# Performance work log

Hardware: AMD Instinct MI355X
Metric: run time of the kernel (lower is better)

Reference implementation:

```python
import jax, jax.numpy as jnp
import numpy as np

EPS = 1e-5


def _forward(fov, motion, video, timewindow,
             gru_w_ih, gru_w_hh, gru_b_ih, gru_b_hh,
             Wp, Wv_w, Wv_b, Wpv_w, Wpv_b,
             conv_w, conv_b, vbn_g, vbn_b,
             me_w, me_b, mbn_g, mbn_b):
    B, S, _ = fov.shape
    P = timewindow.shape[0]
    tot = B * S * P
    H = 784

    # ---- GRU (batch_first, 1 layer), PyTorch gate order r,z,n ----
    def step(h, x):  # h,x: [B,H],[B,528]
        gi = x @ gru_w_ih.T + gru_b_ih            # [B,3H]
        gh = h @ gru_w_hh.T + gru_b_hh
        i_r, i_z, i_n = jnp.split(gi, 3, axis=-1)
        h_r, h_z, h_n = jnp.split(gh, 3, axis=-1)
        r = jax.nn.sigmoid(i_r + h_r)
        z = jax.nn.sigmoid(i_z + h_z)
        n = jnp.tanh(i_n + r * h_n)
        h_new = (1.0 - z) * n + z * h
        return h_new, h_new

    h0 = jnp.zeros((B, H), dtype=fov.dtype)
    _, pref_seq = jax.lax.scan(step, h0, jnp.swapaxes(fov, 0, 1))  # [S,B,H]
    preference = jnp.swapaxes(pref_seq, 0, 1)                       # [B,S,H]

    # expand over P predictions -> [tot, 784]
    preference = jnp.broadcast_to(preference[:, :, None, :], (B, S, P, H)).reshape(tot, H)

    # ---- additive (Bahdanau) attention over 196 spatial locations ----
    p_att = preference @ Wp.T                                       # [tot,128]
    # attention keys: view video buffer as (tot,528,196), transpose
    v_key = jnp.swapaxes(video.reshape(tot, 528, 196), -2, -1)      # [tot,196,528]
    v_att = jnp.einsum('tnc,mc->tnm', v_key, Wv_w) + Wv_b           # [tot,196,128]
    v_att = jnp.tanh(v_att + p_att[:, None, :])
    scores = jnp.einsum('tnm,om->tno', v_att, Wpv_w)[..., 0] + Wpv_b[0]  # [tot,196]
    att = jax.nn.softmax(scores, axis=1)[..., None]                 # [tot,196,1]

    # weighted sum path: SAME buffer reinterpreted as (tot,196,528) (faithful to torch .view)
    vid = video.reshape(tot, 196, 528) * att                        # [tot,196,528]
    vid = jnp.swapaxes(vid, -2, -1)                                 # [tot,528,196]

    # 1x1 conv (528->4) + BatchNorm2d (batch stats) + ReLU
    vid = jnp.einsum('oc,tcn->ton', conv_w[:, :, 0, 0], vid) + conv_b[None, :, None]  # [tot,4,196]
    mu = jnp.mean(vid, axis=(0, 2), keepdims=True)
    var = jnp.var(vid, axis=(0, 2), keepdims=True)
    vid = (vid - mu) * jax.lax.rsqrt(var + EPS) * vbn_g[None, :, None] + vbn_b[None, :, None]
    vid = jax.nn.relu(vid).reshape(tot, 4 * 196)                    # [tot,784]

    # ---- motion branch: expand over P, Linear(90,128) + BatchNorm1d + ReLU ----
    mot = jnp.broadcast_to(motion[:, :, None, :, :], (B, S, P, 1, 90)).reshape(tot, 90)
    mot = mot @ me_w.T + me_b                                       # [tot,128]
    mmu = jnp.mean(mot, axis=0, keepdims=True)
    mvar = jnp.var(mot, axis=0, keepdims=True)
    mot = (mot - mmu) * jax.lax.rsqrt(mvar + EPS) * mbn_g + mbn_b
    mot = jax.nn.relu(mot)                                          # [tot,128]

    tw = jnp.broadcast_to(timewindow[None, :], (B * S, P)).reshape(tot, 1)
    return jnp.concatenate([tw, preference, mot, vid], axis=1)      # [tot,1697]


def setup_inputs() -> dict:
    key = jax.random.key(0)
    ks = jax.random.split(key, 24)
    B, S, P = 8, 32, 5
    C, H, M = 528, 784, 128

    def rn(k, shape, scale=0.05):
        return jax.random.normal(k, shape, dtype=jnp.float32) * scale

    return {
        'fov': rn(ks[0], (B, S, C), 1.0),
        'motion': rn(ks[1], (B, S, 1, 90), 1.0),
        'video': rn(ks[2], (B, S, P, C, 196), 1.0),
        'timewindow': jnp.arange(1, P + 1, dtype=jnp.float32),
        'gru_w_ih': rn(ks[3], (3 * H, C)),
        'gru_w_hh': rn(ks[4], (3 * H, H)),
        'gru_b_ih': rn(ks[5], (3 * H,)),
        'gru_b_hh': rn(ks[6], (3 * H,)),
        'Wp': rn(ks[7], (M, H)),
        'Wv_w': rn(ks[8], (M, C)),
        'Wv_b': rn(ks[9], (M,)),
        'Wpv_w': rn(ks[10], (1, M)),
        'Wpv_b': rn(ks[11], (1,)),
        'conv_w': rn(ks[12], (4, C, 1, 1)),
        'conv_b': rn(ks[13], (4,)),
        'vbn_g': jnp.ones((4,), jnp.float32),
        'vbn_b': jnp.zeros((4,), jnp.float32),
        'me_w': rn(ks[14], (M, 90)),
        'me_b': rn(ks[15], (M,)),
        'mbn_g': jnp.ones((M,), jnp.float32),
        'mbn_b': jnp.zeros((M,), jnp.float32),
    }


def reference(fov, motion, video, timewindow,
              gru_w_ih, gru_w_hh, gru_b_ih, gru_b_hh,
              Wp, Wv_w, Wv_b, Wpv_w, Wpv_b,
              conv_w, conv_b, vbn_g, vbn_b,
              me_w, me_b, mbn_g, mbn_b):
    return _forward(fov, motion, video, timewindow,
                    gru_w_ih, gru_w_hh, gru_b_ih, gru_b_hh,
                    Wp, Wv_w, Wv_b, Wpv_w, Wpv_b,
                    conv_w, conv_b, vbn_g, vbn_b,
                    me_w, me_b, mbn_g, mbn_b)
```

## Files before the change

### kernel.cpp

```cpp
#include <hip/hip_runtime.h>
#include <cfloat>
#include <cmath>


typedef __attribute__((ext_vector_type(8))) short short8;
typedef __attribute__((ext_vector_type(4))) float f32x4;

__device__ __forceinline__ unsigned bf16r(float f) {
  union { float f; unsigned u; } v;
  v.f = f;
  unsigned u = v.u;
  u += 0x7fffu + ((u >> 16) & 1u);
  return u >> 16;
}

__device__ __forceinline__ float tanh_fast(float x) {
  float e = __expf(2.f * x);
  return 1.f - 2.f / (e + 1.f);
}

#define GT_BM 32
#define GT_BN 64
#define GT_BK 16

__global__ __launch_bounds__(256) void gemm_nt(const float* __restrict__ A,
                                               const float* __restrict__ Bt,
                                               const float* __restrict__ bias,
                                               float* __restrict__ Cm,
                                               int Mn, int Nn, int Kn) {
  __shared__ float sA[GT_BM][GT_BK + 1];
  __shared__ float sB[GT_BK][68];
  const int tid = threadIdx.x;
  const int tm = tid >> 4;
  const int tn = tid & 15;
  const int rowBase = blockIdx.y * GT_BM;
  const int colBase = blockIdx.x * GT_BN;
  float acc[2][4] = {};

  for (int k0 = 0; k0 < Kn; k0 += GT_BK) {
    for (int u = tid; u < GT_BM * GT_BK; u += 256) {
      int r = u >> 4, kk = u & 15;
      int gk = k0 + kk, gr = rowBase + r;
      sA[r][kk] = (gr < Mn && gk < Kn) ? A[(size_t)gr * Kn + gk] : 0.f;
    }
    for (int u = tid; u < GT_BN * GT_BK; u += 256) {
      int n = u >> 4, kk = u & 15;
      int gk = k0 + kk, gn = colBase + n;
      sB[kk][n] = (gn < Nn && gk < Kn) ? Bt[(size_t)gn * Kn + gk] : 0.f;
    }
    __syncthreads();
#pragma unroll
    for (int kk = 0; kk < GT_BK; ++kk) {
      float a0 = sA[tm * 2 + 0][kk];
      float a1 = sA[tm * 2 + 1][kk];
      float b0 = sB[kk][tn * 4 + 0];
      float b1 = sB[kk][tn * 4 + 1];
      float b2 = sB[kk][tn * 4 + 2];
      float b3 = sB[kk][tn * 4 + 3];
      acc[0][0] += a0 * b0; acc[0][1] += a0 * b1; acc[0][2] += a0 * b2; acc[0][3] += a0 * b3;
      acc[1][0] += a1 * b0; acc[1][1] += a1 * b1; acc[1][2] += a1 * b2; acc[1][3] += a1 * b3;
    }
    __syncthreads();
  }
#pragma unroll
  for (int i = 0; i < 2; ++i)
#pragma unroll
    for (int j = 0; j < 4; ++j) {
      int gr = rowBase + tm * 2 + i;
      int gc = colBase + tn * 4 + j;
      if (gr < Mn && gc < Nn) {
        float v = acc[i][j];
        if (bias) v += bias[gc];
        Cm[(size_t)gr * Nn + gc] = v;
      }
    }
}

__global__ __launch_bounds__(256) void whh_transpose(const float* __restrict__ W,
                                                     float* __restrict__ WT) {
  __shared__ float tile[32][33];
  const int n0 = blockIdx.x * 32;
  const int k0 = blockIdx.y * 32;
  const int tx = threadIdx.x & 31;
  const int ty = threadIdx.x >> 5;
  for (int i = ty; i < 32; i += 8) {
    int n = n0 + i, k = k0 + tx;
    tile[i][tx] = (n < 2352 && k < 784) ? W[(size_t)n * 784 + k] : 0.f;
  }
  __syncthreads();
  for (int i = ty; i < 32; i += 8) {
    int k = k0 + i, n = n0 + tx;
    if (k < 784 && n < 2352) WT[(size_t)k * 2352 + n] = tile[tx][i];
  }
}

__global__ __launch_bounds__(256) void gru_dots(const float* __restrict__ WT,
                                                const float* __restrict__ h,
                                                float* __restrict__ gh) {
  __shared__ float sh[4 * 784];
  const int tid = threadIdx.x;
  const int bh = blockIdx.y;
  const int bloc = tid >> 6;
  const int b = bh * 4 + bloc;
  const int n = blockIdx.x * 64 + (tid & 63);
  for (int u = tid; u < 3136; u += 256) sh[u] = h[bh * 3136 + u];
  __syncthreads();
  if (n >= 2352) return;
  const float4* h4 = (const float4*)(sh + bloc * 784);
  const float* wp = WT + n;
  float acc = 0.f;
#pragma unroll 2
  for (int kk = 0; kk < 196; ++kk) {
    float4 hv = h4[kk];
    const float* w = wp + (size_t)(kk * 4) * 2352;
    acc += hv.x * w[0];
    acc += hv.y * w[2352];
    acc += hv.z * w[4704];
    acc += hv.w * w[7056];
  }
  gh[b * 2352 + n] = acc;
}

__global__ __launch_bounds__(256) void gru_combine(const float* __restrict__ GI,
                                                   const float* __restrict__ gh,
                                                   const float* __restrict__ bhh,
                                                   const float* __restrict__ h_in,
                                                   float* __restrict__ h_out,
                                                   float* __restrict__ pref,
                                                   int s) {
  const int g = blockIdx.x * 256 + threadIdx.x;
  if (g >= 6272) return;
  const int b = g / 784;
  const int j = g - b * 784;
  const int bs = b * 32 + s;
  const float* gi = GI + (size_t)bs * 2352;
  const float* ghb = gh + b * 2352;
  float ghr = ghb[j] + bhh[j];
  float ghz = ghb[784 + j] + bhh[784 + j];
  float ghn = ghb[1568 + j] + bhh[1568 + j];
  float r = 1.f / (1.f + __expf(-(gi[j] + ghr)));
  float z = 1.f / (1.f + __expf(-(gi[784 + j] + ghz)));
  float nn = tanh_fast(gi[1568 + j] + r * ghn);
  float hn = (1.f - z) * nn + z * h_in[g];
  h_out[g] = hn;
  pref[(size_t)bs * 784 + j] = hn;
}

__global__ __launch_bounds__(128) void mot_stats(const float* __restrict__ mot,
                                                 float* __restrict__ msum,
                                                 float* __restrict__ msq) {
  int m = threadIdx.x;
  float s = 0.f, q = 0.f;
  for (int r = 0; r < 256; ++r) {
    float v = mot[r * 128 + m];
    s += v;
    q += v * v;
  }
  msum[m] = s;
  msq[m] = q;
}

__global__ __launch_bounds__(256, 2) void attn_scores_mfma(
    const float* __restrict__ video, const float* __restrict__ Wv,
    const float* __restrict__ Wvb, const float* __restrict__ patt,
    const float* __restrict__ Wpv, const float* __restrict__ Wpvb,
    float* __restrict__ scores) {
  __shared__ short sA[128 * 40];
  __shared__ short sB[224 * 40];
  __shared__ float pa[128];
  __shared__ float wpv[128];
  __shared__ float ssc[224];

  const int t = blockIdx.x;
  const int bs = t / 5;
  const int tid = threadIdx.x;
  const int wave = tid >> 6;
  const int lane = tid & 63;
  const int q = lane >> 4;
  const int ln = lane & 15;
  const int wm = wave >> 1;
  const int wn = wave & 1;

  if (tid < 128) {
    pa[tid] = Wvb[tid] + patt[(size_t)bs * 128 + tid];
    wpv[tid] = Wpv[tid];
  }
  if (tid < 224) ssc[tid] = 0.f;

  f32x4 acc[4][7];
#pragma unroll
  for (int i = 0; i < 4; ++i)
#pragma unroll
    for (int j = 0; j < 7; ++j) acc[i][j] = (f32x4){0.f, 0.f, 0.f, 0.f};

  const float* vbase = video + (size_t)t * 103488;

  for (int c0 = 0; c0 < 544; c0 += 32) {
    for (int u = tid; u < 2048; u += 256) {
      int m = u >> 4, p = u & 15;
      int c = c0 + 2 * p;
      float f0 = (c < 528) ? Wv[m * 528 + c] : 0.f;
      float f1 = (c + 1 < 528) ? Wv[m * 528 + c + 1] : 0.f;
      unsigned pack = bf16r(f0) | (bf16r(f1) << 16);
      *(unsigned*)&sA[m * 40 + 2 * p] = pack;
    }
    for (int u = tid; u < 3584; u += 256) {
      int p = u / 224;
      int n = u - p * 224;
      int c = c0 + 2 * p;
      float f0 = 0.f, f1 = 0.f;
      if (n < 196) {
        if (c < 528) f0 = vbase[(size_t)c * 196 + n];
        if (c + 1 < 528) f1 = vbase[(size_t)(c + 1) * 196 + n];
      }
      unsigned pack = bf16r(f0) | (bf16r(f1) << 16);
      int pc = p ^ ((n & 3) << 2);
      *(unsigned*)&sB[n * 40 + 2 * pc] = pack;
    }
    __syncthreads();

    short8 afr[4], bfr[7];
#pragma unroll
    for (int mi = 0; mi < 4; ++mi) {
      int m = wm * 64 + mi * 16 + ln;
      afr[mi] = *(const short8*)&sA[m * 40 + q * 8];
    }
#pragma unroll
    for (int nj = 0; nj < 7; ++nj) {
      int n = wn * 112 + nj * 16 + ln;
      int p0 = (q * 4) ^ ((n & 3) << 2);
      bfr[nj] = *(const short8*)&sB[n * 40 + 2 * p0];
    }
#pragma unroll
    for (int mi = 0; mi < 4; ++mi)
#pragma unroll
      for (int nj = 0; nj < 7; ++nj)
        acc[mi][nj] = __builtin_amdgcn_mfma_f32_16x16x32_bf16(
            afr[mi], bfr[nj], acc[mi][nj], 0, 0, 0);
    __syncthreads();
  }

  float contrib[7] = {};
#pragma unroll
  for (int mi = 0; mi < 4; ++mi)
#pragma unroll
    for (int r = 0; r < 4; ++r) {
      int m = wm * 64 + mi * 16 + q * 4 + r;
      float w = wpv[m];
      float bia = pa[m];
#pragma unroll
      for (int nj = 0; nj < 7; ++nj)
        contrib[nj] += w * tanh_fast(acc[mi][nj][r] + bia);
    }
#pragma unroll
  for (int nj = 0; nj < 7; ++nj)
    atomicAdd(&ssc[wn * 112 + nj * 16 + ln], contrib[nj]);
  __syncthreads();
  if (tid < 196) scores[(size_t)t * 196 + tid] = ssc[tid] + Wpvb[0];
}

__global__ __launch_bounds__(256) void attn_conv(
    const float* __restrict__ video, const float* __restrict__ scores,
    const float* __restrict__ convw, const float* __restrict__ convb,
    float* __restrict__ vid_pre, float* __restrict__ vstats) {
  __shared__ float red[256];
  __shared__ float att[196];
  __shared__ float scw[4 * 528];
  __shared__ float pre[784];

  const int t = blockIdx.x;
  const int tid = threadIdx.x;
  for (int u = tid; u < 2112; u += 256) scw[u] = convw[u];

  float v = (tid < 196) ? scores[(size_t)t * 196 + tid] : -FLT_MAX;
  red[tid] = v;
  __syncthreads();
  for (int st = 128; st > 0; st >>= 1) {
    if (tid < st) red[tid] = fmaxf(red[tid], red[tid + st]);
    __syncthreads();
  }
  float mx = red[0];
  __syncthreads();
  float e = (tid < 196) ? __expf(v - mx) : 0.f;
  red[tid] = e;
  __syncthreads();
  for (int st = 128; st > 0; st >>= 1) {
    if (tid < st) red[tid] += red[tid + st];
    __syncthreads();
  }
  float tot = red[0];
  if (tid < 196) att[tid] = e / tot;
  __syncthreads();

  const int lane = tid & 63;
  const int wv = tid >> 6;
  const float* vb = video + (size_t)t * 103488;
  for (int n = wv; n < 196; n += 4) {
    float s0 = 0.f, s1 = 0.f, s2 = 0.f, s3 = 0.f;
    for (int c = lane; c < 528; c += 64) {
      float x = vb[(size_t)n * 528 + c];
      s0 += x * scw[c];
      s1 += x * scw[528 + c];
      s2 += x * scw[1056 + c];
      s3 += x * scw[1584 + c];
    }
#pragma unroll
    for (int off = 32; off > 0; off >>= 1) {
      s0 += __shfl_down(s0, off);
      s1 += __shfl_down(s1, off);
      s2 += __shfl_down(s2, off);
      s3 += __shfl_down(s3, off);
    }
    if (lane == 0) {
      float a = att[n];
      pre[0 * 196 + n] = a * s0 + convb[0];
      pre[1 * 196 + n] = a * s1 + convb[1];
      pre[2 * 196 + n] = a * s2 + convb[2];
      pre[3 * 196 + n] = a * s3 + convb[3];
    }
  }
  __syncthreads();

  float ls[4] = {0.f, 0.f, 0.f, 0.f};
  float lq[4] = {0.f, 0.f, 0.f, 0.f};
  for (int u = tid; u < 784; u += 256) {
    float x = pre[u];
    vid_pre[(size_t)t * 784 + u] = x;
    int o = u / 196;
#pragma unroll
    for (int oo = 0; oo < 4; ++oo) {
      ls[oo] += (o == oo) ? x : 0.f;
      lq[oo] += (o == oo) ? x * x : 0.f;
    }
  }
#pragma unroll
  for (int oo = 0; oo < 4; ++oo)
#pragma unroll
    for (int off = 32; off > 0; off >>= 1) {
      ls[oo] += __shfl_down(ls[oo], off);
      lq[oo] += __shfl_down(lq[oo], off);
    }
  if (lane == 0)
#pragma unroll
    for (int oo = 0; oo < 4; ++oo) {
      atomicAdd(&vstats[oo], ls[oo]);
      atomicAdd(&vstats[4 + oo], lq[oo]);
    }
}

__global__ __launch_bounds__(256) void finalize(
    const float* __restrict__ tw, const float* __restrict__ prefb,
    const float* __restrict__ motl, const float* __restrict__ msum,
    const float* __restrict__ msq, const float* __restrict__ mg,
    const float* __restrict__ mb, const float* __restrict__ vid_pre,
    const float* __restrict__ vstats, const float* __restrict__ vg,
    const float* __restrict__ vbb, float* __restrict__ out) {
  int g = blockIdx.x * 256 + threadIdx.x;
  if (g >= 1280 * 1697) return;
  int t = g / 1697;
  int col = g - t * 1697;
  int bs = t / 5;
  int p = t - bs * 5;
  float r;
  if (col == 0) {
    r = tw[p];
  } else if (col < 785) {
    r = prefb[(size_t)bs * 784 + (col - 1)];
  } else if (col < 913) {
    int m = col - 785;
    float x = motl[(size_t)bs * 128 + m];
    float mu = msum[m] * (1.f / 256.f);
    float var = msq[m] * (1.f / 256.f) - mu * mu;
    float y = (x - mu) * rsqrtf(var + 1e-5f) * mg[m] + mb[m];
    r = fmaxf(y, 0.f);
  } else {
    int qd = col - 913;
    int o = qd / 196;
    float x = vid_pre[(size_t)t * 784 + qd];
    float mu = vstats[o] * (1.f / 250880.f);
    float var = vstats[4 + o] * (1.f / 250880.f) - mu * mu;
    float y = (x - mu) * rsqrtf(var + 1e-5f) * vg[o] + vbb[o];
    r = fmaxf(y, 0.f);
  }
  out[g] = r;
}

extern "C" void kernel_launch(void* const* d_in, const int* in_sizes, int n_in,
                              void* d_out, int out_size, void* d_ws,
                              size_t ws_size, hipStream_t stream) {
  const float* fov = (const float*)d_in[0];
  const float* motion = (const float*)d_in[1];
  const float* video = (const float*)d_in[2];
  const float* timew = (const float*)d_in[3];
  const float* w_ih = (const float*)d_in[4];
  const float* w_hh = (const float*)d_in[5];
  const float* b_ih = (const float*)d_in[6];
  const float* b_hh = (const float*)d_in[7];
  const float* Wp = (const float*)d_in[8];
  const float* Wv_w = (const float*)d_in[9];
  const float* Wv_b = (const float*)d_in[10];
  const float* Wpv_w = (const float*)d_in[11];
  const float* Wpv_b = (const float*)d_in[12];
  const float* conv_w = (const float*)d_in[13];
  const float* conv_b = (const float*)d_in[14];
  const float* vbn_g = (const float*)d_in[15];
  const float* vbn_b = (const float*)d_in[16];
  const float* me_w = (const float*)d_in[17];
  const float* me_b = (const float*)d_in[18];
  const float* mbn_g = (const float*)d_in[19];
  const float* mbn_b = (const float*)d_in[20];

  float* ws = (float*)d_ws;
  float* h0b = ws + 0;
  float* stats = ws + 6272;
  float* msum = stats;
  float* msq = stats + 128;
  float* vstats = stats + 256;
  float* h1b = ws + 6656;
  float* gh = ws + 12928;
  float* GI = ws + 31744;
  float* prefb = ws + 633856;
  float* patt = ws + 834560;
  float* motl = ws + 867328;
  float* scores = ws + 900096;
  float* vid_pre = ws + 1150976;
  float* WT = ws + 2154496;

  hipMemsetAsync(ws, 0, 6536 * sizeof(float), stream);

  whh_transpose<<<dim3(74, 25), 256, 0, stream>>>(w_hh, WT);

  gemm_nt<<<dim3((2352 + GT_BN - 1) / GT_BN, 256 / GT_BM), 256, 0, stream>>>(
      fov, w_ih, b_ih, GI, 256, 2352, 528);

  for (int s = 0; s < 32; ++s) {
    const float* hin = (s & 1) ? h1b : h0b;
    float* hout = (s & 1) ? h0b : h1b;
    gru_dots<<<dim3(37, 2), 256, 0, stream>>>(WT, hin, gh);
    gru_combine<<<25, 256, 0, stream>>>(GI, gh, b_hh, hin, hout, prefb, s);
  }

  gemm_nt<<<dim3(2, 8), 256, 0, stream>>>(prefb, Wp, nullptr, patt, 256, 128, 784);
  gemm_nt<<<dim3(2, 8), 256, 0, stream>>>(motion, me_w, me_b, motl, 256, 128, 90);
  mot_stats<<<1, 128, 0, stream>>>(motl, msum, msq);

  attn_scores_mfma<<<1280, 256, 0, stream>>>(video, Wv_w, Wv_b, patt, Wpv_w,
                                             Wpv_b, scores);
  attn_conv<<<1280, 256, 0, stream>>>(video, scores, conv_w, conv_b, vid_pre,
                                      vstats);

  int total = 1280 * 1697;
  finalize<<<(total + 255) / 256, 256, 0, stream>>>(
      timew, prefb, motl, msum, msq, mbn_g, mbn_b, vid_pre, vstats, vbn_g,
      vbn_b, (float*)d_out);
}
```

Measured before the change: 3.085 ms.

## Fuse attention scoring, softmax and 1x1 conv into one MFMA kernel

Merges the score kernel and the softmax/conv kernel into one kernel per tile. Scores stay in shared memory instead of going through global memory, and shared memory is reused through a union. The 528->4 conv is now done with bf16 MFMA instead of scalar FP32 FMAs, and the second video read uses float4 loads that may hit L2. This drops one launch and the scores round trip. In exchange the conv runs at lower precision (bf16), and most of each 16-row MFMA output tile is wasted because only 4 channels are used. The Wpv bias is dropped because softmax does not change when a constant is added.

```diff
diff --git a/kernel.cpp b/kernel.cpp
--- a/kernel.cpp
+++ b/kernel.cpp
@@ -12,6 +12,13 @@
   unsigned u = v.u;
   u += 0x7fffu + ((u >> 16) & 1u);
   return u >> 16;
+}
+
+__device__ __forceinline__ short8 pack8(const float* f) {
+  short8 r;
+#pragma unroll
+  for (int j = 0; j < 8; ++j) r[j] = (short)bf16r(f[j]);
+  return r;
 }
 
 __device__ __forceinline__ float tanh_fast(float x) {
@@ -160,13 +167,17 @@
   msq[m] = q;
 }
 
-__global__ __launch_bounds__(256, 2) void attn_scores_mfma(
+struct AttnP1 { short sA[128 * 40]; short sB[224 * 40]; };
+struct AttnP2 { float red[256]; float pre[784]; };
+union AttnU { AttnP1 p1; AttnP2 p2; };
+
+__global__ __launch_bounds__(256, 2) void attn_fused(
     const float* __restrict__ video, const float* __restrict__ Wv,
     const float* __restrict__ Wvb, const float* __restrict__ patt,
-    const float* __restrict__ Wpv, const float* __restrict__ Wpvb,
-    float* __restrict__ scores) {
-  __shared__ short sA[128 * 40];
-  __shared__ short sB[224 * 40];
+    const float* __restrict__ Wpv, const float* __restrict__ convw,
+    const float* __restrict__ convb, float* __restrict__ vid_pre,
+    float* __restrict__ vstats) {
+  __shared__ AttnU u;
   __shared__ float pa[128];
   __shared__ float wpv[128];
   __shared__ float ssc[224];
@@ -196,17 +207,17 @@
   const float* vbase = video + (size_t)t * 103488;
 
   for (int c0 = 0; c0 < 544; c0 += 32) {
-    for (int u = tid; u < 2048; u += 256) {
-      int m = u >> 4, p = u & 15;
+    for (int uu = tid; uu < 2048; uu += 256) {
+      int m = uu >> 4, p = uu & 15;
       int c = c0 + 2 * p;
       float f0 = (c < 528) ? Wv[m * 528 + c] : 0.f;
       float f1 = (c + 1 < 528) ? Wv[m * 528 + c + 1] : 0.f;
       unsigned pack = bf16r(f0) | (bf16r(f1) << 16);
-      *(unsigned*)&sA[m * 40 + 2 * p] = pack;
-    }
-    for (int u = tid; u < 3584; u += 256) {
-      int p = u / 224;
-      int n = u - p * 224;
+      *(unsigned*)&u.p1.sA[m * 40 + 2 * p] = pack;
+    }
+    for (int uu = tid; uu < 3584; uu += 256) {
+      int p = uu / 224;
+      int n = uu - p * 224;
       int c = c0 + 2 * p;
       float f0 = 0.f, f1 = 0.f;
       if (n < 196) {
@@ -215,7 +226,7 @@
       }
       unsigned pack = bf16r(f0) | (bf16r(f1) << 16);
       int pc = p ^ ((n & 3) << 2);
-      *(unsigned*)&sB[n * 40 + 2 * pc] = pack;
+      *(unsigned*)&u.p1.sB[n * 40 + 2 * pc] = pack;
     }
     __syncthreads();
 
@@ -223,13 +234,13 @@
 #pragma unroll
     for (int mi = 0; mi < 4; ++mi) {
       int m = wm * 64 + mi * 16 + ln;
-      afr[mi] = *(const short8*)&sA[m * 40 + q * 8];
+      afr[mi] = *(const short8*)&u.p1.sA[m * 40 + q * 8];
     }
 #pragma unroll
     for (int nj = 0; nj < 7; ++nj) {
       int n = wn * 112 + nj * 16 + ln;
       int p0 = (q * 4) ^ ((n & 3) << 2);
-      bfr[nj] = *(const short8*)&sB[n * 40 + 2 * p0];
+      bfr[nj] = *(const short8*)&u.p1.sB[n * 40 + 2 * p0];
     }
 #pragma unroll
     for (int mi = 0; mi < 4; ++mi)
@@ -256,77 +267,74 @@
   for (int nj = 0; nj < 7; ++nj)
     atomicAdd(&ssc[wn * 112 + nj * 16 + ln], contrib[nj]);
   __syncthreads();
-  if (tid < 196) scores[(size_t)t * 196 + tid] = ssc[tid] + Wpvb[0];
-}
-
-__global__ __launch_bounds__(256) void attn_conv(
-    const float* __restrict__ video, const float* __restrict__ scores,
-    const float* __restrict__ convw, const float* __restrict__ convb,
-    float* __restrict__ vid_pre, float* __restrict__ vstats) {
-  __shared__ float red[256];
-  __shared__ float att[196];
-  __shared__ float scw[4 * 528];
-  __shared__ float pre[784];
-
-  const int t = blockIdx.x;
-  const int tid = threadIdx.x;
-  for (int u = tid; u < 2112; u += 256) scw[u] = convw[u];
-
-  float v = (tid < 196) ? scores[(size_t)t * 196 + tid] : -FLT_MAX;
-  red[tid] = v;
+
+  float v = (tid < 196) ? ssc[tid] : -FLT_MAX;
+  u.p2.red[tid] = v;
   __syncthreads();
   for (int st = 128; st > 0; st >>= 1) {
-    if (tid < st) red[tid] = fmaxf(red[tid], red[tid + st]);
-    __syncthreads();
-  }
-  float mx = red[0];
+    if (tid < st) u.p2.red[tid] = fmaxf(u.p2.red[tid], u.p2.red[tid + st]);
+    __syncthreads();
+  }
+  float mx = u.p2.red[0];
   __syncthreads();
   float e = (tid < 196) ? __expf(v - mx) : 0.f;
-  red[tid] = e;
+  u.p2.red[tid] = e;
   __syncthreads();
   for (int st = 128; st > 0; st >>= 1) {
-    if (tid < st) red[tid] += red[tid + st];
-    __syncthreads();
-  }
-  float tot = red[0];
-  if (tid < 196) att[tid] = e / tot;
-  __syncthreads();
-
-  const int lane = tid & 63;
-  const int wv = tid >> 6;
-  const float* vb = video + (size_t)t * 103488;
-  for (int n = wv; n < 196; n += 4) {
-    float s0 = 0.f, s1 = 0.f, s2 = 0.f, s3 = 0.f;
-    for (int c = lane; c < 528; c += 64) {
-      float x = vb[(size_t)n * 528 + c];
-      s0 += x * scw[c];
-      s1 += x * scw[528 + c];
-      s2 += x * scw[1056 + c];
-      s3 += x * scw[1584 + c];
-    }
-#pragma unroll
-    for (int off = 32; off > 0; off >>= 1) {
-      s0 += __shfl_down(s0, off);
-      s1 += __shfl_down(s1, off);
-      s2 += __shfl_down(s2, off);
-      s3 += __shfl_down(s3, off);
-    }
-    if (lane == 0) {
-      float a = att[n];
-      pre[0 * 196 + n] = a * s0 + convb[0];
-      pre[1 * 196 + n] = a * s1 + convb[1];
-      pre[2 * 196 + n] = a * s2 + convb[2];
-      pre[3 * 196 + n] = a * s3 + convb[3];
+    if (tid < st) u.p2.red[tid] += u.p2.red[tid + st];
+    __syncthreads();
+  }
+  float tot = u.p2.red[0];
+  __syncthreads();
+  if (tid < 196) ssc[tid] = e / tot;
+  __syncthreads();
+
+  short8 aw[17];
+#pragma unroll
+  for (int k = 0; k < 17; ++k) {
+    float fa[8];
+#pragma unroll
+    for (int j = 0; j < 8; ++j) {
+      int c = k * 32 + q * 8 + j;
+      fa[j] = (ln < 4 && c < 528) ? convw[ln * 528 + c] : 0.f;
+    }
+    aw[k] = pack8(fa);
+  }
+
+  for (int tile = wave; tile < 13; tile += 4) {
+    int n = tile * 16 + ln;
+    bool nv = (n < 196);
+    const float* vp = vbase + (size_t)n * 528;
+    f32x4 cc = (f32x4){0.f, 0.f, 0.f, 0.f};
+#pragma unroll
+    for (int k = 0; k < 17; ++k) {
+      int c0 = k * 32 + q * 8;
+      short8 bf;
+      if (nv && c0 + 7 < 528) {
+        float4 v0 = *(const float4*)(vp + c0);
+        float4 v1 = *(const float4*)(vp + c0 + 4);
+        float fb[8] = {v0.x, v0.y, v0.z, v0.w, v1.x, v1.y, v1.z, v1.w};
+        bf = pack8(fb);
+      } else {
+        bf = (short8){0, 0, 0, 0, 0, 0, 0, 0};
+      }
+      cc = __builtin_amdgcn_mfma_f32_16x16x32_bf16(aw[k], bf, cc, 0, 0, 0);
+    }
+    if (q == 0 && nv) {
+      float a = ssc[n];
+#pragma unroll
+      for (int r = 0; r < 4; ++r)
+        u.p2.pre[r * 196 + n] = a * cc[r] + convb[r];
     }
   }
   __syncthreads();
 
   float ls[4] = {0.f, 0.f, 0.f, 0.f};
   float lq[4] = {0.f, 0.f, 0.f, 0.f};
-  for (int u = tid; u < 784; u += 256) {
-    float x = pre[u];
-    vid_pre[(size_t)t * 784 + u] = x;
-    int o = u / 196;
+  for (int uu = tid; uu < 784; uu += 256) {
+    float x = u.p2.pre[uu];
+    vid_pre[(size_t)t * 784 + uu] = x;
+    int o = uu / 196;
 #pragma unroll
     for (int oo = 0; oo < 4; ++oo) {
       ls[oo] += (o == oo) ? x : 0.f;
@@ -409,6 +417,7 @@
   const float* me_b = (const float*)d_in[18];
   const float* mbn_g = (const float*)d_in[19];
   const float* mbn_b = (const float*)d_in[20];
+  (void)Wpv_b;
 
   float* ws = (float*)d_ws;
   float* h0b = ws + 0;
@@ -422,7 +431,6 @@
   float* prefb = ws + 633856;
   float* patt = ws + 834560;
   float* motl = ws + 867328;
-  float* scores = ws + 900096;
   float* vid_pre = ws + 1150976;
   float* WT = ws + 2154496;
 
@@ -444,10 +452,8 @@
   gemm_nt<<<dim3(2, 8), 256, 0, stream>>>(motion, me_w, me_b, motl, 256, 128, 90);
   mot_stats<<<1, 128, 0, stream>>>(motl, msum, msq);
 
-  attn_scores_mfma<<<1280, 256, 0, stream>>>(video, Wv_w, Wv_b, patt, Wpv_w,
-                                             Wpv_b, scores);
-  attn_conv<<<1280, 256, 0, stream>>>(video, scores, conv_w, conv_b, vid_pre,
-                                      vstats);
+  attn_fused<<<1280, 256, 0, stream>>>(video, Wv_w, Wv_b, patt, Wpv_w, conv_w,
+                                       conv_b, vid_pre, vstats);
 
   int total = 1280 * 1697;
   finalize<<<(total + 255) / 256, 256, 0, stream>>>(
```

Result: faster. 2.928 ms (-5.1%).
